# Optimization experiments

Hardware: AMD Instinct MI355X
Metric: run time of the kernel (lower is better)

The kernel has to match this reference:

```python
import math
import jax, jax.numpy as jnp
import numpy as np

# ---------- real Wigner 3j (e3nn convention, unit Frobenius norm) ----------
def _su2_cg(j1, j2, j3):
    def f(n):
        return math.factorial(round(n))
    mat = np.zeros((2 * j1 + 1, 2 * j2 + 1, 2 * j3 + 1))
    for m1 in range(-j1, j1 + 1):
        for m2 in range(-j2, j2 + 1):
            m3 = m1 + m2
            if abs(m3) > j3:
                continue
            vmin = max(-j1 + j2 + m3, -j1 + m1, 0)
            vmax = min(j2 + j3 + m1, j3 - j1 + j2, j3 + m3)
            C = math.sqrt((2 * j3 + 1) * f(j3 + j1 - j2) * f(j3 - j1 + j2) * f(j1 + j2 - j3)
                          * f(j3 + m3) * f(j3 - m3)
                          / (f(j1 + j2 + j3 + 1) * f(j1 - m1) * f(j1 + m1) * f(j2 - m2) * f(j2 + m2)))
            S = 0.0
            for v in range(vmin, vmax + 1):
                S += (-1) ** (v + j2 + m2) * f(j2 + j3 + m1 - v) * f(j1 - m1 + v) / (
                    f(v) * f(j3 - j1 + j2 - v) * f(j3 + m3 - v) * f(v + j1 - j2 - m3))
            mat[j1 + m1, j2 + m2, j3 + m3] = C * S
    return mat

def _real_to_complex(l):
    q = np.zeros((2 * l + 1, 2 * l + 1), dtype=np.complex128)
    for m in range(-l, 0):
        q[l + m, l + abs(m)] = 1.0 / math.sqrt(2)
        q[l + m, l - abs(m)] = -1j / math.sqrt(2)
    q[l, l] = 1.0
    for m in range(1, l + 1):
        q[l + m, l + abs(m)] = (-1) ** m / math.sqrt(2)
        q[l + m, l - abs(m)] = 1j * (-1) ** m / math.sqrt(2)
    return (-1j) ** l * q

def _wigner_3j(l1, l2, l3):
    Q1, Q2, Q3 = _real_to_complex(l1), _real_to_complex(l2), _real_to_complex(l3)
    C = _su2_cg(l1, l2, l3).astype(np.complex128)
    C = np.einsum('ij,kl,mn,ikn->jlm', Q1, Q2, np.conj(Q3.T), C).real
    return (C / np.linalg.norm(C)).astype(np.float32)

# ---------- architecture constants (from init_kwargs) ----------
IRREPS_NODE = [(128, 0), (64, 1), (32, 2)]   # 128x0e+64x1e+32x2e, dim 480
IRREPS_EDGE = [(1, 0), (1, 1), (1, 2)]       # 1x0e+1x1e+1x2e (spherical harmonics), dim 9
OUT_LS = (0, 1, 2)
N_NODES, N_EDGES, N_BASIS = 10000, 80000, 128
FC_HIDDEN = 64
AVG_AGG = 8.0
NODE_DIM = sum(m * (2 * l + 1) for m, l in IRREPS_NODE)  # 480

# uvu instructions: (i, l1, j, l2, l3, mul); kept if ir_out in output irreps or 0e
INSTRUCTIONS = []
for _i, (_mul, _l1) in enumerate(IRREPS_NODE):
    for _j, (_, _l2) in enumerate(IRREPS_EDGE):
        for _l3 in range(abs(_l1 - _l2), _l1 + _l2 + 1):
            if _l3 in OUT_LS:
                INSTRUCTIONS.append((_i, _l1, _j, _l2, _l3, _mul))
WEIGHT_NUMEL = sum(ins[5] for ins in INSTRUCTIONS)                       # 960
CAT_MULS = {l: sum(ins[5] for ins in INSTRUCTIONS if ins[4] == l) for l in OUT_LS}  # {0:224,1:384,2:352}
W3J = {(l1, l2, l3): jnp.asarray(_wigner_3j(l1, l2, l3))
       for (_, l1, _, l2, l3, _) in INSTRUCTIONS}

def _layernorm(x, g, b):
    mu = jnp.mean(x, axis=-1, keepdims=True)
    var = jnp.mean((x - mu) ** 2, axis=-1, keepdims=True)
    return (x - mu) * jax.lax.rsqrt(var + 1e-5) * g + b

def _forward(node_input, edge_attr, edge_scalars, edge_src, edge_dst,
             exp_w, exp_b, rad_w1, rad_b1, rad_ln1_g, rad_ln1_b,
             rad_w2, rad_b2, rad_ln2_g, rad_ln2_b, rad_w3, rad_offset,
             proj_w0, proj_w1, proj_w2, proj_b):
    N = node_input.shape[0]
    E = edge_attr.shape[0]
    dt = node_input.dtype
    # exp: LinearRS('1x0e' -> irreps) applied to all-ones scalars; only 0e channels populated
    node0 = jnp.broadcast_to(exp_w + exp_b, (N, IRREPS_NODE[0][0]))   # [N,128]
    xs = [node0[edge_src][:, :, None],                                # [E,128,1] gather by edge_src
          jnp.zeros((E, IRREPS_NODE[1][0], 3), dt),                   # 1e block (structurally zero)
          jnp.zeros((E, IRREPS_NODE[2][0], 5), dt)]                   # 2e block (structurally zero)
    ys = [edge_attr[:, 0:1], edge_attr[:, 1:4], edge_attr[:, 4:9]]
    # radial MLP -> per-edge TP weights [E, 960]
    h = jax.nn.silu(_layernorm(edge_scalars @ rad_w1 + rad_b1, rad_ln1_g, rad_ln1_b))
    h = jax.nn.silu(_layernorm(h @ rad_w2 + rad_b2, rad_ln2_g, rad_ln2_b))
    w = h @ rad_w3 + rad_offset
    # depthwise ('uvu') CG tensor product, outputs grouped by l (even-first sort; all even here)
    per_l = {l: [] for l in OUT_LS}
    off = 0
    for (i, l1, j, l2, l3, mul) in INSTRUCTIONS:
        w_ins = w[:, off:off + mul]   # [E, mul] (v = 1)
        off += mul
        cg = W3J[(l1, l2, l3)] * math.sqrt(2 * l3 + 1)
        per_l[l3].append(jnp.einsum('ijk,eui,ej,eu->euk', cg, xs[i], ys[j], w_ins))
    cat = {l: jnp.concatenate(per_l[l], axis=1) for l in OUT_LS}      # [E, CAT_MULS[l], 2l+1]
    # proj: e3nn Linear (per-l multiplicity mixing; bias on scalars only)
    p0 = jnp.einsum('eui,uo->eoi', cat[0], proj_w0) + proj_b[None, :, None]
    p1 = jnp.einsum('eui,uo->eoi', cat[1], proj_w1)
    p2 = jnp.einsum('eui,uo->eoi', cat[2], proj_w2)
    edge_feat = jnp.concatenate([p0.reshape(E, -1), p1.reshape(E, -1), p2.reshape(E, -1)], axis=1)  # [E,480]
    # scaled scatter-add over destination nodes
    out = jax.ops.segment_sum(edge_feat, edge_dst, num_segments=N)
    return out / math.sqrt(AVG_AGG)

def setup_inputs() -> dict:
    key = jax.random.key(0)
    ks = jax.random.split(key, 16)
    f32 = jnp.float32
    inv = lambda n: 1.0 / math.sqrt(n)
    return {
        'node_input': jax.random.normal(ks[0], (N_NODES, NODE_DIM), f32),
        'edge_attr': jax.random.normal(ks[1], (N_EDGES, 9), f32),
        'edge_scalars': jax.random.uniform(ks[2], (N_EDGES, N_BASIS), f32),
        'edge_src': jax.random.randint(ks[3], (N_EDGES,), 0, N_NODES),
        'edge_dst': jax.random.randint(ks[4], (N_EDGES,), 0, N_NODES),
        'batch': jnp.zeros((N_NODES,), jnp.int32),
        'exp_w': jax.random.normal(ks[5], (128,), f32),
        'exp_b': jnp.zeros((128,), f32),
        'rad_w1': jax.random.normal(ks[6], (N_BASIS, FC_HIDDEN), f32) * inv(N_BASIS),
        'rad_b1': jnp.zeros((FC_HIDDEN,), f32),
        'rad_ln1_g': jnp.ones((FC_HIDDEN,), f32),
        'rad_ln1_b': jnp.zeros((FC_HIDDEN,), f32),
        'rad_w2': jax.random.normal(ks[7], (FC_HIDDEN, FC_HIDDEN), f32) * inv(FC_HIDDEN),
        'rad_b2': jnp.zeros((FC_HIDDEN,), f32),
        'rad_ln2_g': jnp.ones((FC_HIDDEN,), f32),
        'rad_ln2_b': jnp.zeros((FC_HIDDEN,), f32),
        'rad_w3': jax.random.normal(ks[8], (FC_HIDDEN, WEIGHT_NUMEL), f32) * inv(FC_HIDDEN),
        'rad_offset': jax.random.normal(ks[9], (WEIGHT_NUMEL,), f32) * 0.1,
        'proj_w0': jax.random.normal(ks[10], (CAT_MULS[0], 128), f32) * inv(CAT_MULS[0]),
        'proj_w1': jax.random.normal(ks[11], (CAT_MULS[1], 64), f32) * inv(CAT_MULS[1]),
        'proj_w2': jax.random.normal(ks[12], (CAT_MULS[2], 32), f32) * inv(CAT_MULS[2]),
        'proj_b': jnp.zeros((128,), f32),
    }

def reference(node_input, edge_attr, edge_scalars, edge_src, edge_dst, batch,
              exp_w, exp_b, rad_w1, rad_b1, rad_ln1_g, rad_ln1_b,
              rad_w2, rad_b2, rad_ln2_g, rad_ln2_b, rad_w3, rad_offset,
              proj_w0, proj_w1, proj_w2, proj_b):
    return _forward(node_input, edge_attr, edge_scalars, edge_src, edge_dst,
                    exp_w, exp_b, rad_w1, rad_b1, rad_ln1_g, rad_ln1_b,
                    rad_w2, rad_b2, rad_ln2_g, rad_ln2_b, rad_w3, rad_offset,
                    proj_w0, proj_w1, proj_w2, proj_b)
```

## Files before the change

kernel.cpp:

```cpp
#include <hip/hip_runtime.h>
#include <math.h>


#define NEDGES 80000
#define NNODES 10000
#define NPAD   10048
#define NB_L0  157
#define NB_L12 313

__device__ __forceinline__ float silu_f(float y) {
    return y / (1.0f + __expf(-y));
}

__global__ __launch_bounds__(256) void precompute_and_hist(
    const float* __restrict__ exp_w, const float* __restrict__ exp_b,
    const float* __restrict__ rad_w3,
    const float* __restrict__ rad_offset,
    const float* __restrict__ proj_w0,
    const float* __restrict__ proj_w1,
    const float* __restrict__ proj_w2,
    float* __restrict__ M, float* __restrict__ cvec,
    const int* __restrict__ edge_dst, int* __restrict__ counts)
{
    if (blockIdx.x >= 65) {
        int b = blockIdx.x - 65;
        for (int e = b * 256 + threadIdx.x; e < NEDGES; e += 100 * 256)
            atomicAdd(&counts[edge_dst[e]], 1);
        return;
    }
    __shared__ float x0[128];
    int t = threadIdx.x;
    if (t < 128) x0[t] = exp_w[t] + exp_b[t];
    __syncthreads();
    if (t >= 224) return;
    int h = blockIdx.x;
    const float* src = (h < 64) ? (rad_w3 + h * 960) : rad_offset;
    float acc = 0.0f;
    if (t < 128) {
#pragma unroll 4
        for (int u = 0; u < 128; ++u) acc += src[u] * x0[u] * proj_w0[u * 128 + t];
    } else if (t < 192) {
        int o = t - 128;
#pragma unroll 4
        for (int u = 0; u < 128; ++u) acc += src[128 + u] * x0[u] * proj_w1[u * 64 + o];
    } else {
        int o = t - 192;
#pragma unroll 4
        for (int u = 0; u < 128; ++u) acc += src[256 + u] * x0[u] * proj_w2[u * 32 + o];
    }
    if (h < 64) M[h * 224 + t] = acc;
    else        cvec[t] = acc;
}

__global__ __launch_bounds__(1024) void scan_counts(
    int* __restrict__ counts, int* __restrict__ offsets)
{
    __shared__ int wsum[16];
    const int t = threadIdx.x;
    const int lane = t & 63, w = t >> 6;
    const int base = t * 10;
    int local[10];
    int s = 0;
#pragma unroll
    for (int i = 0; i < 10; ++i) {
        int idx = base + i;
        int v = (idx < NNODES) ? counts[idx] : 0;
        local[i] = s;
        s += v;
    }
    int incl = s;
#pragma unroll
    for (int off = 1; off < 64; off <<= 1) {
        int up = __shfl_up(incl, off, 64);
        if (lane >= off) incl += up;
    }
    if (lane == 63) wsum[w] = incl;
    __syncthreads();
    if (t < 16) {
        int v = wsum[t];
#pragma unroll
        for (int off = 1; off < 16; off <<= 1) {
            int up = __shfl_up(v, off, 64);
            if (t >= off) v += up;
        }
        wsum[t] = v;
    }
    __syncthreads();
    int wbase = (w == 0) ? 0 : wsum[w - 1];
    int excl = wbase + incl - s;
#pragma unroll
    for (int i = 0; i < 10; ++i) {
        int idx = base + i;
        if (idx < NNODES) {
            offsets[idx] = excl + local[i];
            counts[idx] = 0;
        }
    }
    if (t == 1023) offsets[NNODES] = excl + s;
}

__global__ __launch_bounds__(256) void edge_h2(
    const float* __restrict__ edge_scalars,
    const float* __restrict__ edge_attr,
    const int*   __restrict__ edge_dst,
    const int*   __restrict__ offsets,
    int*         __restrict__ cursor,
    const float* __restrict__ rad_w1,
    const float* __restrict__ rad_b1,
    const float* __restrict__ g1, const float* __restrict__ bt1,
    const float* __restrict__ rad_w2,
    const float* __restrict__ rad_b2,
    const float* __restrict__ g2, const float* __restrict__ bt2,
    float* __restrict__ h2csr,
    float* __restrict__ ya_csr)
{
    __shared__ float S[12288 + 64];
    float* W1s = S;
    float* ES  = S + 8192;
    int*   pos_s = (int*)(S + 12288);

    const int t    = threadIdx.x;
    const int lane = t & 63;
    const int wid  = t >> 6;
    const int er   = lane & 3;
    const int cc   = lane >> 2;
    const int eb   = blockIdx.x * 64;

    {
        const float4* s1 = (const float4*)rad_w1;
        float4* d1 = (float4*)W1s;
#pragma unroll
        for (int i = 0; i < 8; ++i) d1[t + i * 256] = s1[t + i * 256];
    }
    if (t < 64) {
        int e = eb + t;
        int d = edge_dst[e];
        int p = offsets[d] + atomicAdd(&cursor[d], 1);
        pos_s[t] = p;
        const float* ya = edge_attr + (size_t)e * 9;
        float* dst = ya_csr + (size_t)p * 9;
#pragma unroll
        for (int k = 0; k < 9; ++k) dst[k] = ya[k];
    }
    {
        const int re = t >> 2, seg = t & 3;
        const int col = re ^ (seg << 3);
        const float* row = edge_scalars + (size_t)(eb + re) * 128;
#pragma unroll
        for (int q = 0; q < 4; ++q) {
            float4 v = *(const float4*)(row + seg * 16 + q * 4);
            ES[(seg * 16 + q * 4 + 0) * 64 + col] = v.x;
            ES[(seg * 16 + q * 4 + 1) * 64 + col] = v.y;
            ES[(seg * 16 + q * 4 + 2) * 64 + col] = v.z;
            ES[(seg * 16 + q * 4 + 3) * 64 + col] = v.w;
        }
    }
    __syncthreads();

    const int n0 = cc * 4;
    float b1v[4], g1v[4], t1v[4], b2v[4], g2v[4], t2v[4];
#pragma unroll
    for (int j = 0; j < 4; ++j) {
        b1v[j] = rad_b1[n0 + j]; g1v[j] = g1[n0 + j]; t1v[j] = bt1[n0 + j];
        b2v[j] = rad_b2[n0 + j]; g2v[j] = g2[n0 + j]; t2v[j] = bt2[n0 + j];
    }

    float acc[4][4];
#pragma unroll
    for (int i = 0; i < 4; ++i)
#pragma unroll
        for (int j = 0; j < 4; ++j) acc[i][j] = b1v[j];

    const int ecol = wid * 16 + er * 4;

#pragma unroll 8
    for (int k = 0; k < 64; ++k) {
        float4 av = *(const float4*)&ES[k * 64 + (ecol ^ (((k >> 4) & 3) << 3))];
        float4 wv = *(const float4*)&W1s[k * 64 + n0];
        float a4[4] = {av.x, av.y, av.z, av.w};
        float w4[4] = {wv.x, wv.y, wv.z, wv.w};
#pragma unroll
        for (int i = 0; i < 4; ++i)
#pragma unroll
            for (int j = 0; j < 4; ++j) acc[i][j] = fmaf(a4[i], w4[j], acc[i][j]);
    }
    __syncthreads();
    {
        const int re = t >> 2, seg = t & 3;
        const int col = re ^ (seg << 3);
        const float* row = edge_scalars + (size_t)(eb + re) * 128 + 64;
#pragma unroll
        for (int q = 0; q < 4; ++q) {
            float4 v = *(const float4*)(row + seg * 16 + q * 4);
            ES[(seg * 16 + q * 4 + 0) * 64 + col] = v.x;
            ES[(seg * 16 + q * 4 + 1) * 64 + col] = v.y;
            ES[(seg * 16 + q * 4 + 2) * 64 + col] = v.z;
            ES[(seg * 16 + q * 4 + 3) * 64 + col] = v.w;
        }
    }
    __syncthreads();
#pragma unroll 8
    for (int k = 0; k < 64; ++k) {
        float4 av = *(const float4*)&ES[k * 64 + (ecol ^ (((k >> 4) & 3) << 3))];
        float4 wv = *(const float4*)&W1s[(64 + k) * 64 + n0];
        float a4[4] = {av.x, av.y, av.z, av.w};
        float w4[4] = {wv.x, wv.y, wv.z, wv.w};
#pragma unroll
        for (int i = 0; i < 4; ++i)
#pragma unroll
            for (int j = 0; j < 4; ++j) acc[i][j] = fmaf(a4[i], w4[j], acc[i][j]);
    }
    __syncthreads();

    float* H = W1s + wid * 1280;
    {
        float s1i[4], s2i[4];
#pragma unroll
        for (int i = 0; i < 4; ++i) {
            s1i[i] = acc[i][0] + acc[i][1] + acc[i][2] + acc[i][3];
            s2i[i] = acc[i][0] * acc[i][0] + acc[i][1] * acc[i][1]
                   + acc[i][2] * acc[i][2] + acc[i][3] * acc[i][3];
        }
#pragma unroll
        for (int m = 4; m <= 32; m <<= 1) {
#pragma unroll
            for (int i = 0; i < 4; ++i) {
                s1i[i] += __shfl_xor(s1i[i], m, 64);
                s2i[i] += __shfl_xor(s2i[i], m, 64);
            }
        }
#pragma unroll
        for (int i = 0; i < 4; ++i) {
            float mu  = s1i[i] * (1.0f / 64.0f);
            float var = s2i[i] * (1.0f / 64.0f) - mu * mu;
            float rs  = rsqrtf(var + 1e-5f);
#pragma unroll
            for (int j = 0; j < 4; ++j) {
                float y = (acc[i][j] - mu) * rs * g1v[j] + t1v[j];
                H[(n0 + j) * 20 + er * 4 + i] = silu_f(y);
            }
        }
    }

    float acc2[4][4];
#pragma unroll
    for (int i = 0; i < 4; ++i)
#pragma unroll
        for (int j = 0; j < 4; ++j) acc2[i][j] = b2v[j];
#pragma unroll 8
    for (int u = 0; u < 64; ++u) {
        float4 hv = *(const float4*)&H[u * 20 + er * 4];
        float4 wv = *(const float4*)&rad_w2[u * 64 + n0];
        float h4[4] = {hv.x, hv.y, hv.z, hv.w};
        float w4[4] = {wv.x, wv.y, wv.z, wv.w};
#pragma unroll
        for (int i = 0; i < 4; ++i)
#pragma unroll
            for (int j = 0; j < 4; ++j) acc2[i][j] = fmaf(h4[i], w4[j], acc2[i][j]);
    }

    {
        float s1i[4], s2i[4];
#pragma unroll
        for (int i = 0; i < 4; ++i) {
            s1i[i] = acc2[i][0] + acc2[i][1] + acc2[i][2] + acc2[i][3];
            s2i[i] = acc2[i][0] * acc2[i][0] + acc2[i][1] * acc2[i][1]
                   + acc2[i][2] * acc2[i][2] + acc2[i][3] * acc2[i][3];
        }
#pragma unroll
        for (int m = 4; m <= 32; m <<= 1) {
#pragma unroll
            for (int i = 0; i < 4; ++i) {
                s1i[i] += __shfl_xor(s1i[i], m, 64);
                s2i[i] += __shfl_xor(s2i[i], m, 64);
            }
        }
#pragma unroll
        for (int i = 0; i < 4; ++i) {
            float mu  = s1i[i] * (1.0f / 64.0f);
            float var = s2i[i] * (1.0f / 64.0f) - mu * mu;
            float rs  = rsqrtf(var + 1e-5f);
            float4 v;
            v.x = silu_f((acc2[i][0] - mu) * rs * g2v[0] + t2v[0]);
            v.y = silu_f((acc2[i][1] - mu) * rs * g2v[1] + t2v[1]);
            v.z = silu_f((acc2[i][2] - mu) * rs * g2v[2] + t2v[2]);
            v.w = silu_f((acc2[i][3] - mu) * rs * g2v[3] + t2v[3]);
            *(float4*)&ES[(wid * 16 + er * 4 + i) * 64 + n0] = v;
        }
    }
    __syncthreads();

    {
        const int r = t >> 2, p = t & 3;
        int pos = pos_s[r];
        float* dst = h2csr + (size_t)pos * 64 + p * 16;
        const float* src = &ES[r * 64 + p * 16];
#pragma unroll
        for (int q = 0; q < 4; ++q)
            *(float4*)(dst + q * 4) = *(const float4*)(src + q * 4);
    }
}

__global__ __launch_bounds__(1024) void t_build(
    const float* __restrict__ h2csr,
    const float* __restrict__ ya_csr,
    const int*   __restrict__ offsets,
    float* __restrict__ Tbuf,
    float* __restrict__ ysb)
{
    const int lane = threadIdx.x & 63;
    const int n = __builtin_amdgcn_readfirstlane(blockIdx.x * 16 + (threadIdx.x >> 6));
    const int s0 = offsets[n], s1 = offsets[n + 1];

    float T[9]  = {0, 0, 0, 0, 0, 0, 0, 0, 0};
    float ys[9] = {0, 0, 0, 0, 0, 0, 0, 0, 0};
    for (int i = s0; i < s1; ++i) {
        float hv = h2csr[(size_t)i * 64 + lane];
        const float* ya = ya_csr + (size_t)i * 9;
#pragma unroll
        for (int k = 0; k < 9; ++k) {
            float y = ya[k];
            T[k] += hv * y;
            ys[k] += y;
        }
    }
    float* tb = Tbuf + (size_t)n * 576;
#pragma unroll
    for (int k = 0; k < 9; ++k) tb[k * 64 + lane] = T[k];
#pragma unroll
    for (int k = 0; k < 9; ++k) if (lane == k) ysb[n * 9 + k] = ys[k];
}

__global__ __launch_bounds__(256) void proj(
    const float* __restrict__ Tbuf, const float* __restrict__ ysb,
    const int*   __restrict__ offsets,
    const float* __restrict__ M,
    const float* __restrict__ cvec,
    const float* __restrict__ proj_b,
    float* __restrict__ out)
{
    __shared__ float S[13248];
    const int tid = threadIdx.x;
    const int bid = blockIdx.x;
    constexpr float inv = 0.35355339059327373f;

    if (bid < NB_L0) {
        const int n0 = bid * 64;
        for (int it = tid; it < 1024; it += 256) {
            int ni = it >> 4, q4 = it & 15;
            float4 v = *(const float4*)&Tbuf[(size_t)(n0 + ni) * 576 + q4 * 4];
            S[(q4 * 4 + 0) * 66 + ni] = v.x;
            S[(q4 * 4 + 1) * 66 + ni] = v.y;
            S[(q4 * 4 + 2) * 66 + ni] = v.z;
            S[(q4 * 4 + 3) * 66 + ni] = v.w;
        }
        for (int it = tid; it < 2048; it += 256) {
            int u = it >> 5, c4 = it & 31;
            *(float4*)&S[4224 + u * 128 + c4 * 4] = *(const float4*)&M[u * 224 + c4 * 4];
        }
        __syncthreads();
        const int np = tid & 15, cg = tid >> 4;
        float acc[4][8];
#pragma unroll
        for (int i = 0; i < 4; ++i)
#pragma unroll
            for (int j = 0; j < 8; ++j) acc[i][j] = 0.0f;
#pragma unroll 4
        for (int u = 0; u < 64; ++u) {
            float4 tv = *(const float4*)&S[u * 66 + np * 4];
            float4 m0 = *(const float4*)&S[4224 + u * 128 + cg * 8];
            float4 m1 = *(const float4*)&S[4224 + u * 128 + cg * 8 + 4];
            float ta[4] = {tv.x, tv.y, tv.z, tv.w};
            float ma[8] = {m0.x, m0.y, m0.z, m0.w, m1.x, m1.y, m1.z, m1.w};
#pragma unroll
            for (int i = 0; i < 4; ++i)
#pragma unroll
                for (int j = 0; j < 8; ++j) acc[i][j] = fmaf(ta[i], ma[j], acc[i][j]);
        }
#pragma unroll
        for (int i = 0; i < 4; ++i) {
            int n = n0 + np * 4 + i;
            if (n >= NNODES) continue;
            float ys0 = ysb[n * 9];
            float cnt = (float)(offsets[n + 1] - offsets[n]);
            float f[8];
#pragma unroll
            for (int j = 0; j < 8; ++j) {
                int col = cg * 8 + j;
                f[j] = (acc[i][j] + cvec[col] * ys0 + cnt * proj_b[col]) * inv;
            }
            *(float4*)&out[(size_t)n * 480 + cg * 8]     = *(float4*)&f[0];
            *(float4*)&out[(size_t)n * 480 + cg * 8 + 4] = *(float4*)&f[4];
        }
    } else if (bid < NB_L0 + NB_L12) {
        const int n0 = (bid - NB_L0) * 32;
        for (int it = tid; it < 1536; it += 256) {
            int r = it >> 4, q4 = it & 15;
            int kq = r >> 5, ni = r & 31;
            float4 v = *(const float4*)&Tbuf[(size_t)(n0 + ni) * 576 + (1 + kq) * 64 + q4 * 4];
            float* dst = &S[kq * 2176];
            dst[(q4 * 4 + 0) * 34 + ni] = v.x;
            dst[(q4 * 4 + 1) * 34 + ni] = v.y;
            dst[(q4 * 4 + 2) * 34 + ni] = v.z;
            dst[(q4 * 4 + 3) * 34 + ni] = v.w;
        }
        for (int it = tid; it < 1024; it += 256) {
            int u = it >> 4, c4 = it & 15;
            *(float4*)&S[6528 + u * 64 + c4 * 4] = *(const float4*)&M[u * 224 + 128 + c4 * 4];
        }
        __syncthreads();
        const int np = tid & 15, cg = tid >> 4;
        float acc[2][4][3];
#pragma unroll
        for (int i = 0; i < 2; ++i)
#pragma unroll
            for (int j = 0; j < 4; ++j)
#pragma unroll
                for (int kq = 0; kq < 3; ++kq) acc[i][j][kq] = 0.0f;
#pragma unroll 4
        for (int u = 0; u < 64; ++u) {
            float2 t0 = *(const float2*)&S[0 * 2176 + u * 34 + np * 2];
            float2 t1 = *(const float2*)&S[1 * 2176 + u * 34 + np * 2];
            float2 t2 = *(const float2*)&S[2 * 2176 + u * 34 + np * 2];
            float4 m  = *(const float4*)&S[6528 + u * 64 + cg * 4];
            float ma[4] = {m.x, m.y, m.z, m.w};
            float ta[2][3] = {{t0.x, t1.x, t2.x}, {t0.y, t1.y, t2.y}};
#pragma unroll
            for (int i = 0; i < 2; ++i)
#pragma unroll
                for (int j = 0; j < 4; ++j) {
                    acc[i][j][0] = fmaf(ta[i][0], ma[j], acc[i][j][0]);
                    acc[i][j][1] = fmaf(ta[i][1], ma[j], acc[i][j][1]);
                    acc[i][j][2] = fmaf(ta[i][2], ma[j], acc[i][j][2]);
                }
        }
#pragma unroll
        for (int i = 0; i < 2; ++i) {
            int n = n0 + np * 2 + i;
            if (n >= NNODES) continue;
            float y1 = ysb[n * 9 + 1], y2 = ysb[n * 9 + 2], y3 = ysb[n * 9 + 3];
            float f[12];
#pragma unroll
            for (int j = 0; j < 4; ++j) {
                int cc = cg * 4 + j;
                float cv = cvec[128 + cc];
                f[j * 3 + 0] = (acc[i][j][0] + cv * y1) * inv;
                f[j * 3 + 1] = (acc[i][j][1] + cv * y2) * inv;
                f[j * 3 + 2] = (acc[i][j][2] + cv * y3) * inv;
            }
            float* dst = &out[(size_t)n * 480 + 128 + cg * 12];
            *(float4*)(dst + 0) = *(float4*)&f[0];
            *(float4*)(dst + 4) = *(float4*)&f[4];
            *(float4*)(dst + 8) = *(float4*)&f[8];
        }
    } else {
        const int n0 = (bid - NB_L0 - NB_L12) * 32;
        for (int it = tid; it < 2560; it += 256) {
            int r = it >> 4, q4 = it & 15;
            int kq = r >> 5, ni = r & 31;
            float4 v = *(const float4*)&Tbuf[(size_t)(n0 + ni) * 576 + (4 + kq) * 64 + q4 * 4];
            float* dst = &S[kq * 2176];
            dst[(q4 * 4 + 0) * 34 + ni] = v.x;
            dst[(q4 * 4 + 1) * 34 + ni] = v.y;
            dst[(q4 * 4 + 2) * 34 + ni] = v.z;
            dst[(q4 * 4 + 3) * 34 + ni] = v.w;
        }
        for (int it = tid; it < 512; it += 256) {
            int u = it >> 3, c4 = it & 7;
            *(float4*)&S[10880 + u * 32 + c4 * 4] = *(const float4*)&M[u * 224 + 192 + c4 * 4];
        }
        __syncthreads();
        const int np = tid & 15, cg = tid >> 4;
        float acc[2][2][5];
#pragma unroll
        for (int i = 0; i < 2; ++i)
#pragma unroll
            for (int j = 0; j < 2; ++j)
#pragma unroll
                for (int kq = 0; kq < 5; ++kq) acc[i][j][kq] = 0.0f;
#pragma unroll 4
        for (int u = 0; u < 64; ++u) {
            float2 tq[5];
#pragma unroll
            for (int kq = 0; kq < 5; ++kq)
                tq[kq] = *(const float2*)&S[kq * 2176 + u * 34 + np * 2];
            float2 m = *(const float2*)&S[10880 + u * 32 + cg * 2];
            float ma[2] = {m.x, m.y};
#pragma unroll
            for (int i = 0; i < 2; ++i) {
                float ti[5] = {(&tq[0].x)[i], (&tq[1].x)[i], (&tq[2].x)[i],
                               (&tq[3].x)[i], (&tq[4].x)[i]};
#pragma unroll
                for (int j = 0; j < 2; ++j)
#pragma unroll
                    for (int kq = 0; kq < 5; ++kq)
                        acc[i][j][kq] = fmaf(ti[kq], ma[j], acc[i][j][kq]);
            }
        }
#pragma unroll
        for (int i = 0; i < 2; ++i) {
            int n = n0 + np * 2 + i;
            if (n >= NNODES) continue;
            float yk[5];
#pragma unroll
            for (int kq = 0; kq < 5; ++kq) yk[kq] = ysb[n * 9 + 4 + kq];
            float f[10];
#pragma unroll
            for (int j = 0; j < 2; ++j) {
                int cc = cg * 2 + j;
                float cv = cvec[192 + cc];
#pragma unroll
                for (int kq = 0; kq < 5; ++kq)
                    f[j * 5 + kq] = (acc[i][j][kq] + cv * yk[kq]) * inv;
            }
            float* dst = &out[(size_t)n * 480 + 320 + cg * 10];
#pragma unroll
            for (int q = 0; q < 5; ++q)
                *(float2*)(dst + q * 2) = *(float2*)&f[q * 2];
        }
    }
}

extern "C" void kernel_launch(void* const* d_in, const int* in_sizes, int n_in,
                              void* d_out, int out_size, void* d_ws, size_t ws_size,
                              hipStream_t stream)
{
    const float* edge_attr    = (const float*)d_in[1];
    const float* edge_scalars = (const float*)d_in[2];
    const int*   edge_dst     = (const int*)d_in[4];
    const float* exp_w   = (const float*)d_in[6];
    const float* exp_b   = (const float*)d_in[7];
    const float* rad_w1  = (const float*)d_in[8];
    const float* rad_b1  = (const float*)d_in[9];
    const float* g1      = (const float*)d_in[10];
    const float* bt1     = (const float*)d_in[11];
    const float* rad_w2  = (const float*)d_in[12];
    const float* rad_b2  = (const float*)d_in[13];
    const float* g2      = (const float*)d_in[14];
    const float* bt2     = (const float*)d_in[15];
    const float* rad_w3  = (const float*)d_in[16];
    const float* rad_off = (const float*)d_in[17];
    const float* pw0     = (const float*)d_in[18];
    const float* pw1     = (const float*)d_in[19];
    const float* pw2     = (const float*)d_in[20];
    const float* proj_b  = (const float*)d_in[21];

    float* M       = (float*)d_ws;
    float* cvec    = M + 14336;
    float* h2csr   = cvec + 224;
    int*   counts  = (int*)(h2csr + (size_t)NEDGES * 64);
    int*   offsets = counts + NNODES;
    float* ya_csr  = (float*)(offsets + NNODES + 1);
    float* Tbuf    = ya_csr + (size_t)NEDGES * 9;
    float* ysb     = Tbuf + (size_t)NPAD * 576;

    hipMemsetAsync(counts, 0, NNODES * sizeof(int), stream);
    precompute_and_hist<<<165, 256, 0, stream>>>(exp_w, exp_b, rad_w3, rad_off,
        pw0, pw1, pw2, M, cvec, edge_dst, counts);
    scan_counts<<<1, 1024, 0, stream>>>(counts, offsets);
    edge_h2<<<NEDGES / 64, 256, 0, stream>>>(edge_scalars, edge_attr, edge_dst,
        offsets, counts, rad_w1, rad_b1, g1, bt1, rad_w2, rad_b2, g2, bt2,
        h2csr, ya_csr);
    t_build<<<NNODES / 16, 1024, 0, stream>>>(h2csr, ya_csr, offsets, Tbuf, ysb);
    proj<<<NB_L0 + 2 * NB_L12, 256, 0, stream>>>(Tbuf, ysb, offsets,
        M, cvec, proj_b, (float*)d_out);
}
```

Before: 109.2 us.

## Fuse per-node edge aggregation into projection kernel, dropping Tbuf intermediate

Removes the t_build kernel and its Tbuf/ysb global buffers. Each projection block now walks the CSR edges of its nodes directly and accumulates the needed spherical-harmonic components into shared memory. This cuts one launch and the round trip of the intermediate tensor through memory. In exchange, h2csr is read once per irrep-degree block group (three times in total), and each wave walks several nodes serially, so there is less parallel work in flight.

```diff
diff --git a/kernel.cpp b/kernel.cpp
--- a/kernel.cpp
+++ b/kernel.cpp
@@ -4,7 +4,6 @@
 
 #define NEDGES 80000
 #define NNODES 10000
-#define NPAD   10048
 #define NB_L0  157
 #define NB_L12 313
 
@@ -301,38 +300,9 @@
     }
 }
 
-__global__ __launch_bounds__(1024) void t_build(
+__global__ __launch_bounds__(256) void proj_fused(
     const float* __restrict__ h2csr,
     const float* __restrict__ ya_csr,
-    const int*   __restrict__ offsets,
-    float* __restrict__ Tbuf,
-    float* __restrict__ ysb)
-{
-    const int lane = threadIdx.x & 63;
-    const int n = __builtin_amdgcn_readfirstlane(blockIdx.x * 16 + (threadIdx.x >> 6));
-    const int s0 = offsets[n], s1 = offsets[n + 1];
-
-    float T[9]  = {0, 0, 0, 0, 0, 0, 0, 0, 0};
-    float ys[9] = {0, 0, 0, 0, 0, 0, 0, 0, 0};
-    for (int i = s0; i < s1; ++i) {
-        float hv = h2csr[(size_t)i * 64 + lane];
-        const float* ya = ya_csr + (size_t)i * 9;
-#pragma unroll
-        for (int k = 0; k < 9; ++k) {
-            float y = ya[k];
-            T[k] += hv * y;
-            ys[k] += y;
-        }
-    }
-    float* tb = Tbuf + (size_t)n * 576;
-#pragma unroll
-    for (int k = 0; k < 9; ++k) tb[k * 64 + lane] = T[k];
-#pragma unroll
-    for (int k = 0; k < 9; ++k) if (lane == k) ysb[n * 9 + k] = ys[k];
-}
-
-__global__ __launch_bounds__(256) void proj(
-    const float* __restrict__ Tbuf, const float* __restrict__ ysb,
     const int*   __restrict__ offsets,
     const float* __restrict__ M,
     const float* __restrict__ cvec,
@@ -340,23 +310,33 @@
     float* __restrict__ out)
 {
     __shared__ float S[13248];
-    const int tid = threadIdx.x;
-    const int bid = blockIdx.x;
+    const int tid  = threadIdx.x;
+    const int bid  = blockIdx.x;
+    const int lane = tid & 63;
+    const int wid  = tid >> 6;
     constexpr float inv = 0.35355339059327373f;
 
     if (bid < NB_L0) {
         const int n0 = bid * 64;
-        for (int it = tid; it < 1024; it += 256) {
-            int ni = it >> 4, q4 = it & 15;
-            float4 v = *(const float4*)&Tbuf[(size_t)(n0 + ni) * 576 + q4 * 4];
-            S[(q4 * 4 + 0) * 66 + ni] = v.x;
-            S[(q4 * 4 + 1) * 66 + ni] = v.y;
-            S[(q4 * 4 + 2) * 66 + ni] = v.z;
-            S[(q4 * 4 + 3) * 66 + ni] = v.w;
-        }
+        float* ys0_s = S + 12416;
         for (int it = tid; it < 2048; it += 256) {
             int u = it >> 5, c4 = it & 31;
             *(float4*)&S[4224 + u * 128 + c4 * 4] = *(const float4*)&M[u * 224 + c4 * 4];
+        }
+        for (int nn = 0; nn < 16; ++nn) {
+            int ni = (wid << 4) | nn;
+            int n  = n0 + ni;
+            int s0 = 0, s1 = 0;
+            if (n < NNODES) { s0 = offsets[n]; s1 = offsets[n + 1]; }
+            float T0 = 0.0f, ys0 = 0.0f;
+            for (int i = s0; i < s1; ++i) {
+                float hv = h2csr[(size_t)i * 64 + lane];
+                float y0 = ya_csr[(size_t)i * 9];
+                T0 = fmaf(hv, y0, T0);
+                ys0 += y0;
+            }
+            S[lane * 66 + ni] = T0;
+            if (lane == 0) ys0_s[ni] = ys0;
         }
         __syncthreads();
         const int np = tid & 15, cg = tid >> 4;
@@ -379,9 +359,10 @@
         }
 #pragma unroll
         for (int i = 0; i < 4; ++i) {
-            int n = n0 + np * 4 + i;
+            int ni = np * 4 + i;
+            int n = n0 + ni;
             if (n >= NNODES) continue;
-            float ys0 = ysb[n * 9];
+            float ys0 = ys0_s[ni];
             float cnt = (float)(offsets[n + 1] - offsets[n]);
             float f[8];
 #pragma unroll
@@ -394,19 +375,35 @@
         }
     } else if (bid < NB_L0 + NB_L12) {
         const int n0 = (bid - NB_L0) * 32;
-        for (int it = tid; it < 1536; it += 256) {
-            int r = it >> 4, q4 = it & 15;
-            int kq = r >> 5, ni = r & 31;
-            float4 v = *(const float4*)&Tbuf[(size_t)(n0 + ni) * 576 + (1 + kq) * 64 + q4 * 4];
-            float* dst = &S[kq * 2176];
-            dst[(q4 * 4 + 0) * 34 + ni] = v.x;
-            dst[(q4 * 4 + 1) * 34 + ni] = v.y;
-            dst[(q4 * 4 + 2) * 34 + ni] = v.z;
-            dst[(q4 * 4 + 3) * 34 + ni] = v.w;
-        }
+        float* ysl = S + 10624;
         for (int it = tid; it < 1024; it += 256) {
             int u = it >> 4, c4 = it & 15;
             *(float4*)&S[6528 + u * 64 + c4 * 4] = *(const float4*)&M[u * 224 + 128 + c4 * 4];
+        }
+        for (int nn = 0; nn < 8; ++nn) {
+            int ni = (wid << 3) | nn;
+            int n  = n0 + ni;
+            int s0 = 0, s1 = 0;
+            if (n < NNODES) { s0 = offsets[n]; s1 = offsets[n + 1]; }
+            float T1 = 0.0f, T2 = 0.0f, T3 = 0.0f;
+            float y1s = 0.0f, y2s = 0.0f, y3s = 0.0f;
+            for (int i = s0; i < s1; ++i) {
+                float hv = h2csr[(size_t)i * 64 + lane];
+                const float* ya = ya_csr + (size_t)i * 9;
+                float y1 = ya[1], y2 = ya[2], y3 = ya[3];
+                T1 = fmaf(hv, y1, T1);
+                T2 = fmaf(hv, y2, T2);
+                T3 = fmaf(hv, y3, T3);
+                y1s += y1; y2s += y2; y3s += y3;
+            }
+            S[0 * 2176 + lane * 34 + ni] = T1;
+            S[1 * 2176 + lane * 34 + ni] = T2;
+            S[2 * 2176 + lane * 34 + ni] = T3;
+            if (lane == 0) {
+                ysl[ni * 3 + 0] = y1s;
+                ysl[ni * 3 + 1] = y2s;
+                ysl[ni * 3 + 2] = y3s;
+            }
         }
         __syncthreads();
         const int np = tid & 15, cg = tid >> 4;
@@ -436,9 +433,10 @@
         }
 #pragma unroll
         for (int i = 0; i < 2; ++i) {
-            int n = n0 + np * 2 + i;
+            int ni = np * 2 + i;
+            int n = n0 + ni;
             if (n >= NNODES) continue;
-            float y1 = ysb[n * 9 + 1], y2 = ysb[n * 9 + 2], y3 = ysb[n * 9 + 3];
+            float y1 = ysl[ni * 3 + 0], y2 = ysl[ni * 3 + 1], y3 = ysl[ni * 3 + 2];
             float f[12];
 #pragma unroll
             for (int j = 0; j < 4; ++j) {
@@ -455,19 +453,35 @@
         }
     } else {
         const int n0 = (bid - NB_L0 - NB_L12) * 32;
-        for (int it = tid; it < 2560; it += 256) {
-            int r = it >> 4, q4 = it & 15;
-            int kq = r >> 5, ni = r & 31;
-            float4 v = *(const float4*)&Tbuf[(size_t)(n0 + ni) * 576 + (4 + kq) * 64 + q4 * 4];
-            float* dst = &S[kq * 2176];
-            dst[(q4 * 4 + 0) * 34 + ni] = v.x;
-            dst[(q4 * 4 + 1) * 34 + ni] = v.y;
-            dst[(q4 * 4 + 2) * 34 + ni] = v.z;
-            dst[(q4 * 4 + 3) * 34 + ni] = v.w;
-        }
+        float* ysl = S + 12928;
         for (int it = tid; it < 512; it += 256) {
             int u = it >> 3, c4 = it & 7;
             *(float4*)&S[10880 + u * 32 + c4 * 4] = *(const float4*)&M[u * 224 + 192 + c4 * 4];
+        }
+        for (int nn = 0; nn < 8; ++nn) {
+            int ni = (wid << 3) | nn;
+            int n  = n0 + ni;
+            int s0 = 0, s1 = 0;
+            if (n < NNODES) { s0 = offsets[n]; s1 = offsets[n + 1]; }
+            float T[5] = {0, 0, 0, 0, 0};
+            float ys[5] = {0, 0, 0, 0, 0};
+            for (int i = s0; i < s1; ++i) {
+                float hv = h2csr[(size_t)i * 64 + lane];
+                const float* ya = ya_csr + (size_t)i * 9;
+#pragma unroll
+                for (int kq = 0; kq < 5; ++kq) {
+                    float y = ya[4 + kq];
+                    T[kq] = fmaf(hv, y, T[kq]);
+                    ys[kq] += y;
+                }
+            }
+#pragma unroll
+            for (int kq = 0; kq < 5; ++kq)
+                S[kq * 2176 + lane * 34 + ni] = T[kq];
+            if (lane == 0) {
+#pragma unroll
+                for (int kq = 0; kq < 5; ++kq) ysl[ni * 5 + kq] = ys[kq];
+            }
         }
         __syncthreads();
         const int np = tid & 15, cg = tid >> 4;
@@ -499,11 +513,12 @@
         }
 #pragma unroll
         for (int i = 0; i < 2; ++i) {
-            int n = n0 + np * 2 + i;
+            int ni = np * 2 + i;
+            int n = n0 + ni;
             if (n >= NNODES) continue;
             float yk[5];
 #pragma unroll
-            for (int kq = 0; kq < 5; ++kq) yk[kq] = ysb[n * 9 + 4 + kq];
+            for (int kq = 0; kq < 5; ++kq) yk[kq] = ysl[ni * 5 + kq];
             float f[10];
 #pragma unroll
             for (int j = 0; j < 2; ++j) {
@@ -551,8 +566,6 @@
     int*   counts  = (int*)(h2csr + (size_t)NEDGES * 64);
     int*   offsets = counts + NNODES;
     float* ya_csr  = (float*)(offsets + NNODES + 1);
-    float* Tbuf    = ya_csr + (size_t)NEDGES * 9;
-    float* ysb     = Tbuf + (size_t)NPAD * 576;
 
     hipMemsetAsync(counts, 0, NNODES * sizeof(int), stream);
     precompute_and_hist<<<165, 256, 0, stream>>>(exp_w, exp_b, rad_w3, rad_off,
@@ -561,7 +574,6 @@
     edge_h2<<<NEDGES / 64, 256, 0, stream>>>(edge_scalars, edge_attr, edge_dst,
         offsets, counts, rad_w1, rad_b1, g1, bt1, rad_w2, rad_b2, g2, bt2,
         h2csr, ya_csr);
-    t_build<<<NNODES / 16, 1024, 0, stream>>>(h2csr, ya_csr, offsets, Tbuf, ysb);
-    proj<<<NB_L0 + 2 * NB_L12, 256, 0, stream>>>(Tbuf, ysb, offsets,
+    proj_fused<<<NB_L0 + 2 * NB_L12, 256, 0, stream>>>(h2csr, ya_csr, offsets,
         M, cvec, proj_b, (float*)d_out);
 }
```

Result: slower. 137.0 us (+25.4%).
